# Optimization experiments

Hardware: AMD Instinct MI355X
Metric: run time of the kernel (lower is better)

Reference implementation:

```python
import jax, jax.numpy as jnp
import numpy as np

PATCH_SIZE = 16  # init_kwargs patch_size


def setup_inputs() -> dict:
    key = jax.random.key(0)
    k1, k2, k3 = jax.random.split(key, 3)
    B, C, H, W = 128, 3, 224, 224
    n_points = int(H * W * 0.5 / PATCH_SIZE ** 2)  # 98
    imgs = jax.random.normal(k1, (B, C, H, W), dtype=jnp.float32)
    points_x = jax.random.randint(k2, (B, n_points), 0, H - PATCH_SIZE + 1, dtype=jnp.int32)
    points_y = jax.random.randint(k3, (B, n_points), 0, W - PATCH_SIZE + 1, dtype=jnp.int32)
    return {"imgs": imgs, "points_x": points_x, "points_y": points_y}


def reference(imgs, points_x, points_y):
    # imgs: [B, C, H, W]; points_x/points_y: [B, N] top-left corners of P x P patches to zero.
    B, C, H, W = imgs.shape
    P = PATCH_SIZE
    off = jnp.arange(P, dtype=points_x.dtype)
    b = jnp.arange(B)[:, None, None, None]                       # [B,1,1,1]
    xs = points_x[:, :, None, None] + off[None, None, :, None]    # [B,N,P,1]
    ys = points_y[:, :, None, None] + off[None, None, None, :]    # [B,N,1,P]
    # Build occlusion mask once with a single scatter, then apply across channels.
    mask = jnp.zeros((B, H, W), dtype=jnp.bool_).at[b, xs, ys].set(True)  # [B,H,W]
    return jnp.where(mask[:, None, :, :], jnp.zeros((), imgs.dtype), imgs)
```

## Files before the change

kernel.cpp:

```cpp
#include <hip/hip_runtime.h>

#define BB 128
#define CC 3
#define HH 224
#define WW 224
#define PP 16

#define W4 (WW / 4)
#define PER_IMG4 (CC * HH * W4)
#define NCHUNK 7
#define NWORDS (HH * 7)

__global__ __launch_bounds__(256) void occl_fused(
        float4* __restrict__ out, const float4* __restrict__ imgs,
        const int* __restrict__ px, const int* __restrict__ py, int N) {
    __shared__ unsigned int rowbits[NWORDS];
    const int t = threadIdx.x;
    const int b = blockIdx.y;

    for (int i = t; i < NWORDS; i += 256) rowbits[i] = 0u;
    __syncthreads();

    const int nrow = N * PP;
    for (int r = t; r < nrow; r += 256) {
        int p = r >> 4;
        int i = r & (PP - 1);
        int x = px[b * N + p] + i;
        int y = py[b * N + p];
        unsigned long long mm = 0xFFFFull << (y & 31);
        int w0 = x * 7 + (y >> 5);
        atomicOr(&rowbits[w0], (unsigned int)mm);
        unsigned int hi = (unsigned int)(mm >> 32);
        if (hi) atomicOr(&rowbits[w0 + 1], hi);
    }
    __syncthreads();

    const int chunk = PER_IMG4 / NCHUNK;
    int base = blockIdx.x * chunk;
    const float4* __restrict__ src = imgs + (size_t)b * PER_IMG4;
    float4* __restrict__ dst = out + (size_t)b * PER_IMG4;
#pragma unroll 3
    for (int k = 0; k < chunk / 256; ++k) {
        int f = base + k * 256 + t;
        int w4 = f % W4;
        int hh = (f / W4) % HH;
        unsigned int word = rowbits[hh * 7 + (w4 >> 3)];
        unsigned int m4 = (word >> ((w4 & 7) * 4)) & 0xFu;
        float4 v = src[f];
        if (m4) {
            if (m4 & 1u) v.x = 0.f;
            if (m4 & 2u) v.y = 0.f;
            if (m4 & 4u) v.z = 0.f;
            if (m4 & 8u) v.w = 0.f;
        }
        dst[f] = v;
    }
}

extern "C" void kernel_launch(void* const* d_in, const int* in_sizes, int n_in,
                              void* d_out, int out_size, void* d_ws, size_t ws_size,
                              hipStream_t stream) {
    const float* imgs = (const float*)d_in[0];
    const int*   px   = (const int*)d_in[1];
    const int*   py   = (const int*)d_in[2];
    float*       out  = (float*)d_out;

    const int N = in_sizes[1] / BB;

    dim3 grid(NCHUNK, BB);
    occl_fused<<<grid, 256, 0, stream>>>(
        (float4*)out, (const float4*)imgs, px, py, N);
}
```

Baseline: 144.0 us.

## Split mask build into separate kernel and use flat apply with nontemporal stores

Instead of each of the 7 chunk-blocks per image rebuilding the full row bitmask in shared memory, a first kernel builds the mask once per image into workspace. A second, fully flat kernel with one float4 per thread reads the mask word from global memory (L2-cached), applies it, and writes the output with nontemporal stores. This removes redundant atomic mask construction and raises the number of apply blocks for better memory parallelism. The cost is an extra launch, a dependency between the two kernels, and per-element global mask reads.

```diff
diff --git a/kernel.cpp b/kernel.cpp
--- a/kernel.cpp
+++ b/kernel.cpp
@@ -8,15 +8,17 @@
 
 #define W4 (WW / 4)
 #define PER_IMG4 (CC * HH * W4)
-#define NCHUNK 7
 #define NWORDS (HH * 7)
+#define TOTAL4 (BB * PER_IMG4)
 
-__global__ __launch_bounds__(256) void occl_fused(
-        float4* __restrict__ out, const float4* __restrict__ imgs,
+typedef float vfloat4 __attribute__((ext_vector_type(4)));
+
+__global__ __launch_bounds__(256) void occl_build(
+        unsigned int* __restrict__ gmask,
         const int* __restrict__ px, const int* __restrict__ py, int N) {
     __shared__ unsigned int rowbits[NWORDS];
     const int t = threadIdx.x;
-    const int b = blockIdx.y;
+    const int b = blockIdx.x;
 
     for (int i = t; i < NWORDS; i += 256) rowbits[i] = 0u;
     __syncthreads();
@@ -35,26 +37,26 @@
     }
     __syncthreads();
 
-    const int chunk = PER_IMG4 / NCHUNK;
-    int base = blockIdx.x * chunk;
-    const float4* __restrict__ src = imgs + (size_t)b * PER_IMG4;
-    float4* __restrict__ dst = out + (size_t)b * PER_IMG4;
-#pragma unroll 3
-    for (int k = 0; k < chunk / 256; ++k) {
-        int f = base + k * 256 + t;
-        int w4 = f % W4;
-        int hh = (f / W4) % HH;
-        unsigned int word = rowbits[hh * 7 + (w4 >> 3)];
-        unsigned int m4 = (word >> ((w4 & 7) * 4)) & 0xFu;
-        float4 v = src[f];
-        if (m4) {
-            if (m4 & 1u) v.x = 0.f;
-            if (m4 & 2u) v.y = 0.f;
-            if (m4 & 4u) v.z = 0.f;
-            if (m4 & 8u) v.w = 0.f;
-        }
-        dst[f] = v;
-    }
+    unsigned int* dst = gmask + (size_t)b * NWORDS;
+    for (int i = t; i < NWORDS; i += 256) dst[i] = rowbits[i];
+}
+
+__global__ __launch_bounds__(256) void occl_apply(
+        vfloat4* __restrict__ out, const vfloat4* __restrict__ imgs,
+        const unsigned int* __restrict__ gmask) {
+    int f = blockIdx.x * 256 + threadIdx.x;
+    int w4 = f % W4;
+    int t  = f / W4;
+    int h  = t % HH;
+    int b  = t / (HH * CC);
+    unsigned int word = gmask[(size_t)b * NWORDS + h * 7 + (w4 >> 3)];
+    unsigned int m4 = (word >> ((w4 & 7) * 4)) & 0xFu;
+    vfloat4 v = imgs[f];
+    if (m4 & 1u) v.x = 0.f;
+    if (m4 & 2u) v.y = 0.f;
+    if (m4 & 4u) v.z = 0.f;
+    if (m4 & 8u) v.w = 0.f;
+    __builtin_nontemporal_store(v, &out[f]);
 }
 
 extern "C" void kernel_launch(void* const* d_in, const int* in_sizes, int n_in,
@@ -67,7 +69,7 @@
 
     const int N = in_sizes[1] / BB;
 
-    dim3 grid(NCHUNK, BB);
-    occl_fused<<<grid, 256, 0, stream>>>(
-        (float4*)out, (const float4*)imgs, px, py, N);
+    occl_build<<<BB, 256, 0, stream>>>((unsigned int*)d_ws, px, py, N);
+    occl_apply<<<TOTAL4 / 256, 256, 0, stream>>>(
+        (vfloat4*)out, (const vfloat4*)imgs, (const unsigned int*)d_ws);
 }
```

After: 139.3 us. 1.03x faster.
